# Performance work log

Hardware: AMD Instinct MI355X
Metric: run time of the kernel (lower is better)

The kernel has to match this reference:

```python
import jax, jax.numpy as jnp
import numpy as np

BITS, NF, NX = 8, 4096, 1024
G = NX // 8  # groups of 8 weights packed per uint8


def setup_inputs() -> dict:
    key = jax.random.key(0)
    k1, k2, k3, k4 = jax.random.split(key, 4)
    x = jax.random.normal(k1, (2, 2048, NX), dtype=jnp.float32)
    # packed sign bytes per (bit-plane, out-feature, group-of-8 inputs)
    binary = jax.random.randint(k2, (BITS, NF, G), 0, 256, dtype=jnp.int32)
    # per-bit-plane, per-output-row scale (always positive in the sup/l2 schemes)
    scale = jax.random.uniform(k3, (BITS, NF, 1), dtype=jnp.float32)
    bias = jax.random.normal(k4, (NF,), dtype=jnp.float32)
    return {"x": x, "binary": binary, "scale": scale, "bias": bias}


def _decode_signs(binary):
    # binary_exp in the torch code is [2^7..2^0], so element j of each group of 8
    # is stored in bit (7 - j). map4 maps a set bit -> +1, clear bit -> -1.
    shifts = jnp.arange(7, -1, -1, dtype=binary.dtype)
    bits = (binary[..., None] >> shifts) & 1  # (BITS, NF, G, 8)
    sign = jnp.where(bits == 1, 1.0, -1.0).astype(jnp.float32)
    return sign.reshape(binary.shape[0], binary.shape[1], -1)  # (BITS, NF, NX)


def reference(x, binary, scale, bias):
    # Math of the original forward:
    #   table[t, g, hi, lo] = x[t, 8g:8g+4] . map4[:, hi] + x[t, 8g+4:8g+8] . map4[:, lo]
    #   out[t, f] = sum_i scale[i, f] * sum_g table[t, g, binary[i,f,g]>>4, binary[i,f,g]&15]
    # which is exactly sum_i scale[i,f] * (x[t] . sign_i[f]).  We fold the
    # bit-plane sum into an effective weight and run one dense GEMM.
    size_out = x.shape[:-1] + (scale.shape[1],)
    xf = x.reshape(-1, x.shape[-1])            # (T, NX)
    sign = _decode_signs(binary)               # (BITS, NF, NX), values in {-1,+1}
    W = jnp.einsum('kfn,kfo->fn', sign, scale)  # effective weight (NF, NX)
    out = xf @ W.T + bias                      # (T, NF)
    return out.reshape(size_out)
```

## Files before the change

kernel.cpp:

```cpp
#include <hip/hip_runtime.h>
#include <hip/hip_bf16.h>
#include <stdint.h>


#define BITS 8
#define NF   4096
#define NXX  1024
#define GRP  (NXX / 8)

#define BM 128
#define BN 256
#define BK 64

typedef __attribute__((ext_vector_type(4))) float f32x4;
typedef __attribute__((ext_vector_type(8))) short bf16x8;

__global__ __launch_bounds__(256) void k_prep(const float* __restrict__ x,
                                              const int* __restrict__ binary,
                                              const float* __restrict__ scale,
                                              __hip_bfloat16* __restrict__ xb,
                                              __hip_bfloat16* __restrict__ Wb) {
    const int b = blockIdx.x;
    const int tid = threadIdx.x;
    if (b < 2048) {
        int i = b * 256 + tid;
        const float4* xp = (const float4*)x;
        float4 a = xp[2 * i], c = xp[2 * i + 1];
        union { __hip_bfloat16 h[8]; int4 v; } u;
        u.h[0] = __float2bfloat16(a.x);
        u.h[1] = __float2bfloat16(a.y);
        u.h[2] = __float2bfloat16(a.z);
        u.h[3] = __float2bfloat16(a.w);
        u.h[4] = __float2bfloat16(c.x);
        u.h[5] = __float2bfloat16(c.y);
        u.h[6] = __float2bfloat16(c.z);
        u.h[7] = __float2bfloat16(c.w);
        ((int4*)xb)[i] = u.v;
    } else {
        int idx = (b - 2048) * 256 + tid;
        int f = idx >> 7;
        int g = idx & (GRP - 1);
        float sc[BITS];
        int   bv[BITS];
#pragma unroll
        for (int k = 0; k < BITS; ++k) {
            sc[k] = scale[k * NF + f];
            bv[k] = binary[(size_t)(k * NF + f) * GRP + g];
        }
        union { __hip_bfloat16 h[8]; int4 v; } u;
#pragma unroll
        for (int j = 0; j < 8; ++j) {
            float s = 0.f;
#pragma unroll
            for (int k = 0; k < BITS; ++k)
                s += ((bv[k] >> (7 - j)) & 1) ? sc[k] : -sc[k];
            u.h[j] = __float2bfloat16(s);
        }
        ((int4*)Wb)[idx] = u.v;
    }
}

__global__ __launch_bounds__(256, 2) void k_gemm(const __hip_bfloat16* __restrict__ A,
                                                 const __hip_bfloat16* __restrict__ B,
                                                 const float* __restrict__ bias,
                                                 float* __restrict__ C,
                                                 int M, int N, int K) {
    __shared__ __align__(16) char lds[49152];

    const int tid  = threadIdx.x;
    const int lane = tid & 63;
    const int wv   = tid >> 6;
    const int lr = lane & 15;
    const int lk = lane >> 4;

    const int bid = blockIdx.x;
    const int swz = (bid & 7) * 64 + (bid >> 3);
    const int m0 = (swz & 31) * BM;
    const int n0 = (swz >> 5) * BN;

    const int NT = K / BK;

    int offA[4], dstA[4], offB[8], dstB[8];
#pragma unroll
    for (int j = 0; j < 4; ++j) {
        int c = j * 256 + tid, r = c >> 3, q = c & 7;
        offA[j] = r * K + (q ^ (r & 7)) * 8;
        dstA[j] = c * 16;
    }
#pragma unroll
    for (int j = 0; j < 8; ++j) {
        int c = j * 256 + tid, r = c >> 3, q = c & 7;
        offB[j] = r * K + (q ^ (r & 7)) * 8;
        dstB[j] = 16384 + c * 16;
    }
    const __hip_bfloat16* Abase = A + (size_t)m0 * K;
    const __hip_bfloat16* Bbase = B + (size_t)n0 * K;

    auto stage = [&](int kt) {
#pragma unroll
        for (int j = 0; j < 4; ++j)
            __builtin_amdgcn_global_load_lds(
                (const __attribute__((address_space(1))) void*)(Abase + offA[j] + kt),
                (__attribute__((address_space(3))) void*)(lds + dstA[j]), 16, 0, 0);
#pragma unroll
        for (int j = 0; j < 8; ++j)
            __builtin_amdgcn_global_load_lds(
                (const __attribute__((address_space(1))) void*)(Bbase + offB[j] + kt),
                (__attribute__((address_space(3))) void*)(lds + dstB[j]), 16, 0, 0);
    };
    auto ldA = [&](int i, int kk) -> bf16x8 {
        int R = i * 16 + lr;
        int CB = (kk * 64 + lk * 16) ^ ((R & 7) << 4);
        return *(const bf16x8*)(lds + R * 128 + CB);
    };
    auto ldB = [&](int j, int kk) -> bf16x8 {
        int R = wv * 64 + j * 16 + lr;
        int CB = (kk * 64 + lk * 16) ^ ((R & 7) << 4);
        return *(const bf16x8*)(lds + 16384 + R * 128 + CB);
    };

    f32x4 acc[8][4] = {};
    bf16x8 aF[4][2], bF[4][2];

    stage(0);
    for (int t = 0; t < NT; ++t) {
        __syncthreads();
#pragma unroll
        for (int j = 0; j < 4; ++j) { bF[j][0] = ldB(j, 0); bF[j][1] = ldB(j, 1); }
#pragma unroll
        for (int i = 0; i < 4; ++i) { aF[i][0] = ldA(i, 0); aF[i][1] = ldA(i, 1); }
        __builtin_amdgcn_s_setprio(1);
#pragma unroll
        for (int i = 0; i < 4; ++i)
#pragma unroll
            for (int j = 0; j < 4; ++j)
#pragma unroll
                for (int kk = 0; kk < 2; ++kk)
                    acc[i][j] = __builtin_amdgcn_mfma_f32_16x16x32_bf16(
                        aF[i][kk], bF[j][kk], acc[i][j], 0, 0, 0);
        __builtin_amdgcn_s_setprio(0);
#pragma unroll
        for (int i = 0; i < 4; ++i) { aF[i][0] = ldA(4 + i, 0); aF[i][1] = ldA(4 + i, 1); }
        __syncthreads();
        if (t + 1 < NT) stage((t + 1) * BK);
        __builtin_amdgcn_s_setprio(1);
#pragma unroll
        for (int i = 0; i < 4; ++i)
#pragma unroll
            for (int j = 0; j < 4; ++j)
#pragma unroll
                for (int kk = 0; kk < 2; ++kk)
                    acc[4 + i][j] = __builtin_amdgcn_mfma_f32_16x16x32_bf16(
                        aF[i][kk], bF[j][kk], acc[4 + i][j], 0, 0, 0);
        __builtin_amdgcn_s_setprio(0);
    }

#pragma unroll
    for (int j = 0; j < 4; ++j) {
        int col = n0 + wv * 64 + j * 16 + lr;
        float bv = bias[col];
#pragma unroll
        for (int i = 0; i < 8; ++i) {
            int row = m0 + i * 16 + lk * 4;
#pragma unroll
            for (int r = 0; r < 4; ++r)
                C[(size_t)(row + r) * N + col] = acc[i][j][r] + bv;
        }
    }
}

extern "C" void kernel_launch(void* const* d_in, const int* in_sizes, int n_in,
                              void* d_out, int out_size, void* d_ws, size_t ws_size,
                              hipStream_t stream) {
    const float* x      = (const float*)d_in[0];
    const int*   binary = (const int*)d_in[1];
    const float* scale  = (const float*)d_in[2];
    const float* bias   = (const float*)d_in[3];
    float* out = (float*)d_out;

    const int M = in_sizes[0] / NXX;

    __hip_bfloat16* xb = (__hip_bfloat16*)d_ws;
    __hip_bfloat16* Wb = xb + (size_t)M * NXX;

    k_prep<<<2048 + (NF * GRP) / 256, 256, 0, stream>>>(x, binary, scale, xb, Wb);
    k_gemm<<<(M / BM) * (NF / BN), 256, 0, stream>>>(xb, Wb, bias, out, M, NF, NXX);
}
```

Before: 131.7 us.

## Load A fragments directly from global into registers and double-buffer B in LDS

```diff
diff --git a/kernel.cpp b/kernel.cpp
--- a/kernel.cpp
+++ b/kernel.cpp
@@ -65,7 +65,7 @@
                                                  const float* __restrict__ bias,
                                                  float* __restrict__ C,
                                                  int M, int N, int K) {
-    __shared__ __align__(16) char lds[49152];
+    __shared__ __align__(16) char lds[65536];
 
     const int tid  = threadIdx.x;
     const int lane = tid & 63;
@@ -80,55 +80,66 @@
 
     const int NT = K / BK;
 
-    int offA[4], dstA[4], offB[8], dstB[8];
-#pragma unroll
-    for (int j = 0; j < 4; ++j) {
-        int c = j * 256 + tid, r = c >> 3, q = c & 7;
-        offA[j] = r * K + (q ^ (r & 7)) * 8;
-        dstA[j] = c * 16;
-    }
+    int offB[8], dstB[8];
 #pragma unroll
     for (int j = 0; j < 8; ++j) {
         int c = j * 256 + tid, r = c >> 3, q = c & 7;
         offB[j] = r * K + (q ^ (r & 7)) * 8;
-        dstB[j] = 16384 + c * 16;
-    }
-    const __hip_bfloat16* Abase = A + (size_t)m0 * K;
+        dstB[j] = c * 16;
+    }
     const __hip_bfloat16* Bbase = B + (size_t)n0 * K;
-
-    auto stage = [&](int kt) {
-#pragma unroll
-        for (int j = 0; j < 4; ++j)
-            __builtin_amdgcn_global_load_lds(
-                (const __attribute__((address_space(1))) void*)(Abase + offA[j] + kt),
-                (__attribute__((address_space(3))) void*)(lds + dstA[j]), 16, 0, 0);
+    const __hip_bfloat16* Aptr = A + (size_t)(m0 + lr) * K + lk * 8;
+
+    auto stageB = [&](int buf, int kt) {
 #pragma unroll
         for (int j = 0; j < 8; ++j)
             __builtin_amdgcn_global_load_lds(
                 (const __attribute__((address_space(1))) void*)(Bbase + offB[j] + kt),
-                (__attribute__((address_space(3))) void*)(lds + dstB[j]), 16, 0, 0);
-    };
-    auto ldA = [&](int i, int kk) -> bf16x8 {
-        int R = i * 16 + lr;
-        int CB = (kk * 64 + lk * 16) ^ ((R & 7) << 4);
-        return *(const bf16x8*)(lds + R * 128 + CB);
-    };
-    auto ldB = [&](int j, int kk) -> bf16x8 {
+                (__attribute__((address_space(3))) void*)(lds + buf * 32768 + dstB[j]), 16, 0, 0);
+    };
+    auto ldB = [&](int buf, int j, int kk) -> bf16x8 {
         int R = wv * 64 + j * 16 + lr;
         int CB = (kk * 64 + lk * 16) ^ ((R & 7) << 4);
-        return *(const bf16x8*)(lds + 16384 + R * 128 + CB);
+        return *(const bf16x8*)(lds + buf * 32768 + R * 128 + CB);
     };
 
     f32x4 acc[8][4] = {};
-    bf16x8 aF[4][2], bF[4][2];
-
-    stage(0);
+    bf16x8 aFa[4][2], aFb[4][2], bF[4][2];
+
+    auto loadAa = [&](int kt) {
+#pragma unroll
+        for (int i = 0; i < 4; ++i)
+#pragma unroll
+            for (int kk = 0; kk < 2; ++kk)
+                aFa[i][kk] = *(const bf16x8*)(Aptr + (size_t)(i * 16) * K + kt + kk * 32);
+    };
+    auto loadAb = [&](int kt) {
+#pragma unroll
+        for (int i = 0; i < 4; ++i)
+#pragma unroll
+            for (int kk = 0; kk < 2; ++kk)
+                aFb[i][kk] = *(const bf16x8*)(Aptr + (size_t)((i + 4) * 16) * K + kt + kk * 32);
+    };
+
+    stageB(0, 0);
+    __builtin_amdgcn_sched_barrier(0);
+    loadAa(0);
+    __builtin_amdgcn_sched_barrier(0);
+    loadAb(0);
+    __builtin_amdgcn_sched_barrier(0);
+
     for (int t = 0; t < NT; ++t) {
-        __syncthreads();
-#pragma unroll
-        for (int j = 0; j < 4; ++j) { bF[j][0] = ldB(j, 0); bF[j][1] = ldB(j, 1); }
-#pragma unroll
-        for (int i = 0; i < 4; ++i) { aF[i][0] = ldA(i, 0); aF[i][1] = ldA(i, 1); }
+        const int cb = t & 1;
+        const bool st = (t + 1 < NT);
+        asm volatile("s_waitcnt vmcnt(16)" ::: "memory");
+        __builtin_amdgcn_s_barrier();
+        __builtin_amdgcn_sched_barrier(0);
+
+#pragma unroll
+        for (int j = 0; j < 4; ++j) { bF[j][0] = ldB(cb, j, 0); bF[j][1] = ldB(cb, j, 1); }
+        if (st) stageB(cb ^ 1, (t + 1) * BK);
+        __builtin_amdgcn_sched_barrier(0);
+
         __builtin_amdgcn_s_setprio(1);
 #pragma unroll
         for (int i = 0; i < 4; ++i)
@@ -137,12 +148,12 @@
 #pragma unroll
                 for (int kk = 0; kk < 2; ++kk)
                     acc[i][j] = __builtin_amdgcn_mfma_f32_16x16x32_bf16(
-                        aF[i][kk], bF[j][kk], acc[i][j], 0, 0, 0);
+                        aFa[i][kk], bF[j][kk], acc[i][j], 0, 0, 0);
         __builtin_amdgcn_s_setprio(0);
-#pragma unroll
-        for (int i = 0; i < 4; ++i) { aF[i][0] = ldA(4 + i, 0); aF[i][1] = ldA(4 + i, 1); }
-        __syncthreads();
-        if (t + 1 < NT) stage((t + 1) * BK);
+        __builtin_amdgcn_sched_barrier(0);
+        if (st) loadAa((t + 1) * BK);
+        __builtin_amdgcn_sched_barrier(0);
+
         __builtin_amdgcn_s_setprio(1);
 #pragma unroll
         for (int i = 0; i < 4; ++i)
@@ -151,8 +162,11 @@
 #pragma unroll
                 for (int kk = 0; kk < 2; ++kk)
                     acc[4 + i][j] = __builtin_amdgcn_mfma_f32_16x16x32_bf16(
-                        aF[i][kk], bF[j][kk], acc[4 + i][j], 0, 0, 0);
+                        aFb[i][kk], bF[j][kk], acc[4 + i][j], 0, 0, 0);
         __builtin_amdgcn_s_setprio(0);
+        __builtin_amdgcn_sched_barrier(0);
+        if (st) loadAb((t + 1) * BK);
+        __builtin_amdgcn_sched_barrier(0);
     }
 
 #pragma unroll
```

After: 201.2 us. +52.8%, slower.

## Double-buffer B tile in LDS and issue next-tile loads earlier

Applied to the files above, without the earlier changes.

```diff
diff --git a/kernel.cpp b/kernel.cpp
--- a/kernel.cpp
+++ b/kernel.cpp
@@ -65,7 +65,7 @@
                                                  const float* __restrict__ bias,
                                                  float* __restrict__ C,
                                                  int M, int N, int K) {
-    __shared__ __align__(16) char lds[49152];
+    __shared__ __align__(16) char lds[81920];
 
     const int tid  = threadIdx.x;
     const int lane = tid & 63;
@@ -80,55 +80,66 @@
 
     const int NT = K / BK;
 
-    int offA[4], dstA[4], offB[8], dstB[8];
+    int offA[4], offB[8];
 #pragma unroll
     for (int j = 0; j < 4; ++j) {
         int c = j * 256 + tid, r = c >> 3, q = c & 7;
         offA[j] = r * K + (q ^ (r & 7)) * 8;
-        dstA[j] = c * 16;
     }
 #pragma unroll
     for (int j = 0; j < 8; ++j) {
         int c = j * 256 + tid, r = c >> 3, q = c & 7;
         offB[j] = r * K + (q ^ (r & 7)) * 8;
-        dstB[j] = 16384 + c * 16;
     }
     const __hip_bfloat16* Abase = A + (size_t)m0 * K;
     const __hip_bfloat16* Bbase = B + (size_t)n0 * K;
 
-    auto stage = [&](int kt) {
+    auto stageA = [&](int kt) {
 #pragma unroll
         for (int j = 0; j < 4; ++j)
             __builtin_amdgcn_global_load_lds(
                 (const __attribute__((address_space(1))) void*)(Abase + offA[j] + kt),
-                (__attribute__((address_space(3))) void*)(lds + dstA[j]), 16, 0, 0);
+                (__attribute__((address_space(3))) void*)(lds + (j * 256 + tid) * 16), 16, 0, 0);
+    };
+    auto stageB = [&](int buf, int kt) {
 #pragma unroll
         for (int j = 0; j < 8; ++j)
             __builtin_amdgcn_global_load_lds(
                 (const __attribute__((address_space(1))) void*)(Bbase + offB[j] + kt),
-                (__attribute__((address_space(3))) void*)(lds + dstB[j]), 16, 0, 0);
+                (__attribute__((address_space(3))) void*)(lds + 16384 + buf * 32768 + (j * 256 + tid) * 16), 16, 0, 0);
     };
     auto ldA = [&](int i, int kk) -> bf16x8 {
         int R = i * 16 + lr;
         int CB = (kk * 64 + lk * 16) ^ ((R & 7) << 4);
         return *(const bf16x8*)(lds + R * 128 + CB);
     };
-    auto ldB = [&](int j, int kk) -> bf16x8 {
+    auto ldB = [&](int buf, int j, int kk) -> bf16x8 {
         int R = wv * 64 + j * 16 + lr;
         int CB = (kk * 64 + lk * 16) ^ ((R & 7) << 4);
-        return *(const bf16x8*)(lds + 16384 + R * 128 + CB);
+        return *(const bf16x8*)(lds + 16384 + buf * 32768 + R * 128 + CB);
     };
 
     f32x4 acc[8][4] = {};
-    bf16x8 aF[4][2], bF[4][2];
-
-    stage(0);
+    bf16x8 aF[4][2], aG[4][2], bF[4][2];
+
+    stageA(0);
+    stageB(0, 0);
+
     for (int t = 0; t < NT; ++t) {
-        __syncthreads();
-#pragma unroll
-        for (int j = 0; j < 4; ++j) { bF[j][0] = ldB(j, 0); bF[j][1] = ldB(j, 1); }
+        const int cb = t & 1;
+        const bool st = (t + 1 < NT);
+        asm volatile("s_waitcnt vmcnt(0)" ::: "memory");
+        __builtin_amdgcn_s_barrier();
+
+        if (st) stageB(cb ^ 1, (t + 1) * BK);
+
 #pragma unroll
         for (int i = 0; i < 4; ++i) { aF[i][0] = ldA(i, 0); aF[i][1] = ldA(i, 1); }
+#pragma unroll
+        for (int j = 0; j < 4; ++j) { bF[j][0] = ldB(cb, j, 0); bF[j][1] = ldB(cb, j, 1); }
+#pragma unroll
+        for (int i = 0; i < 4; ++i) { aG[i][0] = ldA(4 + i, 0); aG[i][1] = ldA(4 + i, 1); }
+
         __builtin_amdgcn_s_setprio(1);
 #pragma unroll
         for (int i = 0; i < 4; ++i)
@@ -139,10 +150,11 @@
                     acc[i][j] = __builtin_amdgcn_mfma_f32_16x16x32_bf16(
                         aF[i][kk], bF[j][kk], acc[i][j], 0, 0, 0);
         __builtin_amdgcn_s_setprio(0);
-#pragma unroll
-        for (int i = 0; i < 4; ++i) { aF[i][0] = ldA(4 + i, 0); aF[i][1] = ldA(4 + i, 1); }
-        __syncthreads();
-        if (t + 1 < NT) stage((t + 1) * BK);
+
+        asm volatile("s_waitcnt lgkmcnt(0)" ::: "memory");
+        __builtin_amdgcn_s_barrier();
+        if (st) stageA((t + 1) * BK);
+
         __builtin_amdgcn_s_setprio(1);
 #pragma unroll
         for (int i = 0; i < 4; ++i)
@@ -151,7 +163,7 @@
 #pragma unroll
                 for (int kk = 0; kk < 2; ++kk)
                     acc[4 + i][j] = __builtin_amdgcn_mfma_f32_16x16x32_bf16(
-                        aF[i][kk], bF[j][kk], acc[4 + i][j], 0, 0, 0);
+                        aG[i][kk], bF[j][kk], acc[4 + i][j], 0, 0, 0);
         __builtin_amdgcn_s_setprio(0);
     }
 
```

New measurement: 133.7 us. Within noise of the previous version (+1.5%).
